# Kernel optimization log

Hardware: AMD Instinct MI355X
Metric: run time of the kernel (lower is better)

Reference implementation:

```python
import jax, jax.numpy as jnp
import numpy as np

B, H, E = 8192, 1024, 8


def setup_inputs() -> dict:
    key = jax.random.key(0)
    ks = jax.random.split(key, 6)
    scale = 0.02  # keep gate/expert logits in a sane range
    return {
        "x": jax.random.normal(ks[0], (B, H), jnp.float32),
        "class_label": jax.random.randint(ks[1], (B,), 0, 2),
        "gate_w": jax.random.normal(ks[2], (E, H), jnp.float32) * scale,
        "w1": jax.random.normal(ks[3], (E, H, H), jnp.float32) * scale,
        "b1": jnp.zeros((E, H), jnp.float32),
        "w2": jax.random.normal(ks[4], (E, H, 2), jnp.float32) * scale,
        "b2": jnp.zeros((E, 2), jnp.float32),
    }


def reference(x, class_label, gate_w, w1, b1, w2, b2):
    num_experts = w1.shape[0]
    # --- router ---
    logits = x @ gate_w.T                              # [B, E]
    routing_prob = jax.nn.softmax(logits, axis=-1)     # [B, E]
    idx = jnp.argmax(routing_prob, axis=-1)            # [B] top-1 expert
    dispatch_onehot = jax.nn.one_hot(idx, num_experts, dtype=jnp.float32)
    balancing_loss = (routing_prob.mean(axis=0) * dispatch_onehot.mean(axis=0)).sum() * num_experts
    router_z_loss = jnp.mean(jax.nn.logsumexp(logits, axis=-1) ** 2)
    # --- experts: compute all experts densely, then select the routed one ---
    h = jax.nn.gelu(jnp.einsum('bh,ehd->bed', x, w1) + b1[None], approximate=False)  # [B, E, H]
    probs = jax.nn.softmax(jnp.einsum('bed,edc->bec', h, w2) + b2[None], axis=-1)    # [B, E, 2]
    expert_out = jnp.take_along_axis(probs, idx[:, None, None], axis=1)[:, 0, :]     # [B, 2]
    # --- straight-through-style weight: value 1, grad flows through p_max ---
    p_max = routing_prob.max(axis=-1)                  # [B]
    weight = p_max + jax.lax.stop_gradient(1.0 - p_max)
    weighted_logits = expert_out * weight[:, None]     # [B, 2]
    # CrossEntropyLoss applied on (already softmaxed) outputs, faithful to source
    logp = jax.nn.log_softmax(weighted_logits, axis=-1)
    ce_loss = -jnp.take_along_axis(logp, class_label[:, None], axis=1).mean()
    loss = ce_loss + 0.01 * balancing_loss + 0.001 * router_z_loss
    return loss
```

## Files before the change

kernel.cpp:

```cpp
#include <hip/hip_runtime.h>
#include <math.h>

#define BQ 8192
#define HD 1024
#define NE 8
#define CAP 1280

#define BM 256
#define BN 128
#define BK 64
#define NRT 5
#define TILES_PER_E 40


#define WS_CURSOR   0
#define WS_TICK     32
#define WS_S        64
#define WS_ZSUM     96
#define WS_CESUM    100
#define WS_ROWLIST  128
#define WS_LOGITS2  41088
#define WS_HEAD     123008
#define WS_XC       123008
#define WS_W1T      10608768

using f32x4  = __attribute__((ext_vector_type(4))) float;

__device__ __forceinline__ float gelu_exact(float v) {
    return 0.5f * v * (1.0f + erff(v * 0.70710678118654752440f));
}

__device__ __forceinline__ unsigned int f4_to_fp8x4(float f0, float f1, float f2, float f3) {
    int lo = __builtin_amdgcn_cvt_pk_fp8_f32(f0, f1, 0, false);
    return (unsigned int)__builtin_amdgcn_cvt_pk_fp8_f32(f2, f3, lo, true);
}

__device__ __forceinline__ void gll16(const void* g, void* l) {
    __builtin_amdgcn_global_load_lds((const __attribute__((address_space(1))) void*)g,
                                     (__attribute__((address_space(3))) void*)l, 16, 0, 0);
}

__global__ __launch_bounds__(256) void prep_kernel(
    const float* __restrict__ x, const float* __restrict__ gate_w,
    const float* __restrict__ w1,
    int* __restrict__ cursor, float* __restrict__ S, float* __restrict__ zsum,
    int* __restrict__ rowlist, unsigned char* __restrict__ xcq,
    unsigned char* __restrict__ w1tq)
{
    __shared__ __align__(16) char smem[33280];
    int tid = threadIdx.x;

    if (blockIdx.x >= 256) {
        char (*lt)[80] = (char (*)[80])smem;
        int tile = blockIdx.x - 256;
        int e = tile >> 8;
        int rem = tile & 255;
        int k0 = (rem >> 4) << 6, n0 = (rem & 15) << 6;
        const float* src = w1 + ((size_t)e << 20) + (size_t)k0 * HD + n0;
        #pragma unroll
        for (int s = 0; s < 4; s++) {
            int q = tid + s * 256;
            int kk = q >> 4, n4 = q & 15;
            float4 v = *(const float4*)(src + (size_t)kk * HD + n4 * 4);
            unsigned int b = f4_to_fp8x4(v.x * 8.f, v.y * 8.f, v.z * 8.f, v.w * 8.f);
            lt[n4 * 4 + 0][kk] = (char)(b);
            lt[n4 * 4 + 1][kk] = (char)(b >> 8);
            lt[n4 * 4 + 2][kk] = (char)(b >> 16);
            lt[n4 * 4 + 3][kk] = (char)(b >> 24);
        }
        __syncthreads();
        int nn = tid >> 2, q = tid & 3;
        int pos0 = ((q & 1) << 5) | ((q >> 1) << 3);
        unsigned char* dst = w1tq + ((size_t)e << 20) + (size_t)(n0 + nn) * HD + k0;
        const unsigned long long* sp = (const unsigned long long*)&lt[nn][q * 16];
        *(unsigned long long*)(dst + pos0)      = sp[0];
        *(unsigned long long*)(dst + pos0 + 16) = sp[1];
        return;
    }

    float* gw    = (float*)smem;
    float* sS    = (float*)(smem + 32768);
    float* sZ    = (float*)(smem + 32800);
    int*   sBI   = (int*)(smem + 32832);
    int*   sSlot = (int*)(smem + 32960);
    int*   sBase = (int*)(smem + 33088);

    for (int i = tid * 4; i < NE * HD; i += 256 * 4) {
        *(float4*)(gw + i) = *(const float4*)(gate_w + i);
    }
    if (tid < NE) sS[tid] = 0.f;
    if (tid == 0) sZ[0] = 0.f;
    __syncthreads();

    int wave = tid >> 6, lane = tid & 63;
    int r0 = blockIdx.x * 32;
    float accS[NE];
    #pragma unroll
    for (int e = 0; e < NE; e++) accS[e] = 0.f;
    float accZ = 0.f;

    #pragma unroll 1
    for (int i = 0; i < 8; i++) {
        int li = wave * 8 + i;
        int r = r0 + li;
        const float* xr = x + (size_t)r * HD;
        float acc[NE];
        #pragma unroll
        for (int e = 0; e < NE; e++) acc[e] = 0.f;
        #pragma unroll
        for (int it = 0; it < 4; it++) {
            int k = lane * 4 + it * 256;
            float4 xv = *(const float4*)(xr + k);
            #pragma unroll
            for (int e = 0; e < NE; e++) {
                const float* g = gw + e * HD + k;
                acc[e] += xv.x * g[0] + xv.y * g[1] + xv.z * g[2] + xv.w * g[3];
            }
        }
        #pragma unroll
        for (int e = 0; e < NE; e++) {
            #pragma unroll
            for (int off = 32; off > 0; off >>= 1)
                acc[e] += __shfl_xor(acc[e], off);
        }
        if (lane == 0) {
            float m = acc[0]; int bi = 0;
            #pragma unroll
            for (int e = 1; e < NE; e++) if (acc[e] > m) { m = acc[e]; bi = e; }
            float se = 0.f, ex[NE];
            #pragma unroll
            for (int e = 0; e < NE; e++) { ex[e] = expf(acc[e] - m); se += ex[e]; }
            float inv = 1.f / se;
            #pragma unroll
            for (int e = 0; e < NE; e++) accS[e] += ex[e] * inv;
            float lse = m + logf(se);
            accZ += lse * lse;
            sBI[li] = bi;
        }
    }
    if (lane == 0) {
        #pragma unroll
        for (int e = 0; e < NE; e++) atomicAdd(&sS[e], accS[e]);
        atomicAdd(sZ, accZ);
    }
    __syncthreads();

    if (tid < NE) {
        int cnt = 0;
        #pragma unroll
        for (int j = 0; j < 32; j++) cnt += (sBI[j] == tid);
        sBase[tid] = atomicAdd(&cursor[tid], cnt);
        atomicAdd(&S[tid], sS[tid]);
    }
    if (tid == 0) atomicAdd(zsum, sZ[0]);
    __syncthreads();

    if (tid < 32) {
        int bi = sBI[tid];
        int rank = 0;
        for (int j = 0; j < tid; j++) rank += (sBI[j] == bi);
        int slot = sBase[bi] + rank;
        sSlot[tid] = slot;
        if (slot < CAP) rowlist[bi * CAP + slot] = r0 + tid;
    }
    __syncthreads();

    #pragma unroll 1
    for (int i = 0; i < 8; i++) {
        int li = wave * 8 + i;
        int bi = sBI[li];
        int pos = sSlot[li];
        if (pos >= CAP) continue;
        const float* src = x + (size_t)(r0 + li) * HD + lane * 16;
        float4 v0 = *(const float4*)(src + 0);
        float4 v1 = *(const float4*)(src + 4);
        float4 v2 = *(const float4*)(src + 8);
        float4 v3 = *(const float4*)(src + 12);
        unsigned int g0a = f4_to_fp8x4(v0.x, v0.y, v0.z, v0.w);
        unsigned int g0b = f4_to_fp8x4(v1.x, v1.y, v1.z, v1.w);
        unsigned int g1a = f4_to_fp8x4(v2.x, v2.y, v2.z, v2.w);
        unsigned int g1b = f4_to_fp8x4(v3.x, v3.y, v3.z, v3.w);
        int s = lane >> 2, q = lane & 3;
        int pos0 = (s << 6) | ((q & 1) << 5) | ((q >> 1) << 3);
        unsigned char* dst = xcq + ((size_t)(bi * CAP + pos)) * HD;
        *(unsigned long long*)(dst + pos0)      = (unsigned long long)g0a | ((unsigned long long)g0b << 32);
        *(unsigned long long*)(dst + pos0 + 16) = (unsigned long long)g1a | ((unsigned long long)g1b << 32);
    }
}

__global__ __launch_bounds__(512, 4) void expert_gemm_kernel(
    const unsigned char* __restrict__ xcq, const unsigned char* __restrict__ w1tq,
    const float* __restrict__ b1, const float* __restrict__ w2,
    const int* __restrict__ cursor, int* __restrict__ tick,
    float* __restrict__ logits2c)
{
    int e = blockIdx.x & 7;
    int cnt = cursor[e]; if (cnt > CAP) cnt = CAP;

    __shared__ __align__(16) char lds[3][24576];
    __shared__ int sTix;

    int t = threadIdx.x;
    int l = t & 63;
    int scolb = ((t & 3) ^ ((t >> 3) & 3)) << 4;
    int m = t >> 2;

    int wid = t >> 6;
    int wr = wid >> 1, wc = wid & 1;
    int r = l & 15, h = l >> 4;
    int off = (h << 4) ^ (((r >> 1) & 3) << 4);

    const unsigned char* xcp  = xcq + ((size_t)e * CAP) * HD;
    const unsigned char* w1tp = w1tq + ((size_t)e << 20);

    for (;;) {
        if (t == 0) sTix = atomicAdd(&tick[e], 1);
        __syncthreads();
        int tix = sTix;
        if (tix >= TILES_PER_E) break;
        int col = tix / NRT;
        int rt = tix - col * NRT;
        if (rt * BM >= cnt) continue;
        int n0 = col * BN;

        const unsigned char* srcA  = xcp + (size_t)(rt * BM + m) * HD + scolb;
        const unsigned char* srcA1 = srcA + (size_t)128 * HD;
        const unsigned char* srcB  = w1tp + (size_t)(n0 + m) * HD + scolb;

        f32x4 acc[4][4];
        #pragma unroll
        for (int i = 0; i < 4; i++)
            #pragma unroll
            for (int j = 0; j < 4; j++) acc[i][j] = (f32x4)(0.f);

        auto stage = [&](int bi) {
            gll16(srcA,  lds[bi] + t * 16);         srcA  += BK;
            gll16(srcA1, lds[bi] + 8192 + t * 16);  srcA1 += BK;
            gll16(srcB,  lds[bi] + 16384 + t * 16); srcB  += BK;
        };
        auto compute = [&](int bi) {
            const char* Ar = lds[bi] + (wr * 64 + r) * 64 + off;
            const char* Br = lds[bi] + 16384 + (wc * 64 + r) * 64 + off;
            longlong2 av[4], bv[4];
            #pragma unroll
            for (int i = 0; i < 4; i++) {
                av[i] = *(const longlong2*)(Ar + i * 1024);
                bv[i] = *(const longlong2*)(Br + i * 1024);
            }
            #pragma unroll
            for (int i = 0; i < 4; i++)
                #pragma unroll
                for (int j = 0; j < 4; j++)
                    acc[i][j] = __builtin_amdgcn_mfma_f32_16x16x32_fp8_fp8(av[i].x, bv[j].x, acc[i][j], 0, 0, 0);
            #pragma unroll
            for (int i = 0; i < 4; i++)
                #pragma unroll
                for (int j = 0; j < 4; j++)
                    acc[i][j] = __builtin_amdgcn_mfma_f32_16x16x32_fp8_fp8(av[i].y, bv[j].y, acc[i][j], 0, 0, 0);
        };

        stage(0); stage(1);
        int cs = 2, cc = 0;
        #pragma unroll 1
        for (int it = 0; it < HD / BK - 2; ++it) {
            asm volatile("s_waitcnt vmcnt(3)" ::: "memory");
            __builtin_amdgcn_s_barrier();
            stage(cs); cs = (cs == 2) ? 0 : cs + 1;
            compute(cc); cc = (cc == 2) ? 0 : cc + 1;
        }
        asm volatile("s_waitcnt vmcnt(3)" ::: "memory");
        __builtin_amdgcn_s_barrier();
        compute(cc); cc = (cc == 2) ? 0 : cc + 1;
        asm volatile("s_waitcnt vmcnt(0)" ::: "memory");
        __builtin_amdgcn_s_barrier();
        compute(cc);

        float b1v[4], w20v[4], w21v[4];
        #pragma unroll
        for (int j = 0; j < 4; j++) {
            int cj = n0 + wc * 64 + j * 16 + r;
            b1v[j]  = b1[e * HD + cj];
            w20v[j] = w2[((size_t)e * HD + cj) * 2 + 0];
            w21v[j] = w2[((size_t)e * HD + cj) * 2 + 1];
        }
        #pragma unroll
        for (int i = 0; i < 4; i++) {
            #pragma unroll
            for (int reg = 0; reg < 4; reg++) {
                float s0 = 0.f, s1 = 0.f;
                #pragma unroll
                for (int j = 0; j < 4; j++) {
                    float hv = gelu_exact(acc[i][j][reg] * 0.125f + b1v[j]);
                    s0 += hv * w20v[j];
                    s1 += hv * w21v[j];
                }
                #pragma unroll
                for (int offx = 1; offx < 16; offx <<= 1) {
                    s0 += __shfl_xor(s0, offx);
                    s1 += __shfl_xor(s1, offx);
                }
                if (r == 0) {
                    int lm = wr * 64 + i * 16 + 4 * h + reg;
                    int p = rt * BM + lm;
                    if (p < cnt) {
                        atomicAdd(&logits2c[(e * CAP + p) * 2 + 0], s0);
                        atomicAdd(&logits2c[(e * CAP + p) * 2 + 1], s1);
                    }
                }
            }
        }
    }
}

__global__ __launch_bounds__(256) void ce_kernel(
    const float* __restrict__ logits2c, const float* __restrict__ b2,
    const int* __restrict__ cursor, const int* __restrict__ rowlist,
    const int* __restrict__ label, float* __restrict__ cesum)
{
    __shared__ float red[4];
    int tid = threadIdx.x;
    int s = blockIdx.x * 256 + tid;
    int e = s / CAP;
    int local = s - e * CAP;
    int cnt = cursor[e]; if (cnt > CAP) cnt = CAP;
    float ce = 0.f;
    if (local < cnt) {
        int rr = rowlist[s];
        float l0 = logits2c[s * 2 + 0] + b2[e * 2 + 0];
        float l1 = logits2c[s * 2 + 1] + b2[e * 2 + 1];
        float mx = fmaxf(l0, l1);
        float e0 = expf(l0 - mx), e1 = expf(l1 - mx);
        float inv = 1.f / (e0 + e1);
        float p0 = e0 * inv, p1 = e1 * inv;
        float m2 = fmaxf(p0, p1);
        float z = m2 + logf(expf(p0 - m2) + expf(p1 - m2));
        float lp = ((label[rr] == 0) ? p0 : p1) - z;
        ce = -lp;
    }
    int lane = tid & 63, wave = tid >> 6;
    #pragma unroll
    for (int off = 32; off > 0; off >>= 1) ce += __shfl_xor(ce, off);
    if (lane == 0) red[wave] = ce;
    __syncthreads();
    if (tid == 0) atomicAdd(cesum, red[0] + red[1] + red[2] + red[3]);
}

__global__ void finalize_kernel(const float* __restrict__ S, const int* __restrict__ cursor,
                                const float* __restrict__ zsum, const float* __restrict__ cesum,
                                float* __restrict__ out)
{
    if (threadIdx.x == 0 && blockIdx.x == 0) {
        float bal = 0.f;
        for (int e = 0; e < NE; e++) bal += S[e] * (float)cursor[e];
        bal *= (float)NE / ((float)BQ * (float)BQ);
        out[0] = cesum[0] / (float)BQ + 0.01f * bal + 0.001f * (zsum[0] / (float)BQ);
    }
}

extern "C" void kernel_launch(void* const* d_in, const int* in_sizes, int n_in,
                              void* d_out, int out_size, void* d_ws, size_t ws_size,
                              hipStream_t stream) {
    const float* x      = (const float*)d_in[0];
    const int*   label  = (const int*)d_in[1];
    const float* gate_w = (const float*)d_in[2];
    const float* w1     = (const float*)d_in[3];
    const float* b1     = (const float*)d_in[4];
    const float* w2     = (const float*)d_in[5];
    const float* b2     = (const float*)d_in[6];
    float* out = (float*)d_out;

    char* ws = (char*)d_ws;
    int*   cursor   = (int*)(ws + WS_CURSOR);
    int*   tick     = (int*)(ws + WS_TICK);
    float* S        = (float*)(ws + WS_S);
    float* zsum     = (float*)(ws + WS_ZSUM);
    float* cesum    = (float*)(ws + WS_CESUM);
    int*   rowlist  = (int*)(ws + WS_ROWLIST);
    float* logits2c = (float*)(ws + WS_LOGITS2);
    unsigned char* xcq  = (unsigned char*)(ws + WS_XC);
    unsigned char* w1tq = (unsigned char*)(ws + WS_W1T);

    hipMemsetAsync(d_ws, 0, WS_HEAD, stream);

    prep_kernel<<<2304, 256, 0, stream>>>(x, gate_w, w1, cursor, S, zsum,
                                          rowlist, xcq, w1tq);
    expert_gemm_kernel<<<512, 512, 0, stream>>>(xcq, w1tq, b1, w2, cursor, tick,
                                                logits2c);
    ce_kernel<<<NE * CAP / 256, 256, 0, stream>>>(logits2c, b2, cursor, rowlist,
                                                  label, cesum);
    finalize_kernel<<<1, 64, 0, stream>>>(S, cursor, zsum, cesum, out);
}
```

Measured before the change: 85.71 us.

## Replace persistent atomic tile scheduler with static 128x128 tiles per block

The expert GEMM's row tile shrinks from 256 to 128 and each block drops from 512 to 256 threads. The persistent loop that claimed tiles through an atomic ticket counter is replaced by a static grid of one block per (expert, tile), with blocks that fall past the expert's row count exiting early. This removes the per-tile atomic and barrier and gives finer-grained load balance when experts have uneven row counts. In exchange, each tile reuses less of the loaded data and more blocks must be launched.

```diff
diff --git a/kernel.cpp b/kernel.cpp
--- a/kernel.cpp
+++ b/kernel.cpp
@@ -6,15 +6,15 @@
 #define NE 8
 #define CAP 1280
 
-#define BM 256
+#define BM 128
 #define BN 128
 #define BK 64
-#define NRT 5
-#define TILES_PER_E 40
+#define NRT 10
+#define NCT 8
+#define TILES_PER_E 80
 
 
 #define WS_CURSOR   0
-#define WS_TICK     32
 #define WS_S        64
 #define WS_ZSUM     96
 #define WS_CESUM    100
@@ -188,17 +188,21 @@
     }
 }
 
-__global__ __launch_bounds__(512, 4) void expert_gemm_kernel(
+__global__ __launch_bounds__(256, 3) void expert_gemm_kernel(
     const unsigned char* __restrict__ xcq, const unsigned char* __restrict__ w1tq,
     const float* __restrict__ b1, const float* __restrict__ w2,
-    const int* __restrict__ cursor, int* __restrict__ tick,
-    float* __restrict__ logits2c)
+    const int* __restrict__ cursor, float* __restrict__ logits2c)
 {
-    int e = blockIdx.x & 7;
+    int bid = blockIdx.x;
+    int e = bid & 7;
+    int tix = bid >> 3;
+    int col = tix / NRT;
+    int rt = tix - col * NRT;
     int cnt = cursor[e]; if (cnt > CAP) cnt = CAP;
-
-    __shared__ __align__(16) char lds[3][24576];
-    __shared__ int sTix;
+    if (rt * BM >= cnt) return;
+    int n0 = col * BN;
+
+    __shared__ __align__(16) char lds[3][16384];
 
     int t = threadIdx.x;
     int l = t & 63;
@@ -213,99 +217,89 @@
     const unsigned char* xcp  = xcq + ((size_t)e * CAP) * HD;
     const unsigned char* w1tp = w1tq + ((size_t)e << 20);
 
-    for (;;) {
-        if (t == 0) sTix = atomicAdd(&tick[e], 1);
-        __syncthreads();
-        int tix = sTix;
-        if (tix >= TILES_PER_E) break;
-        int col = tix / NRT;
-        int rt = tix - col * NRT;
-        if (rt * BM >= cnt) continue;
-        int n0 = col * BN;
-
-        const unsigned char* srcA  = xcp + (size_t)(rt * BM + m) * HD + scolb;
-        const unsigned char* srcA1 = srcA + (size_t)128 * HD;
-        const unsigned char* srcB  = w1tp + (size_t)(n0 + m) * HD + scolb;
-
-        f32x4 acc[4][4];
+    const unsigned char* srcA0 = xcp + (size_t)(rt * BM + m) * HD + scolb;
+    const unsigned char* srcA1 = srcA0 + (size_t)64 * HD;
+    const unsigned char* srcB0 = w1tp + (size_t)(n0 + m) * HD + scolb;
+    const unsigned char* srcB1 = srcB0 + (size_t)64 * HD;
+
+    f32x4 acc[4][4];
+    #pragma unroll
+    for (int i = 0; i < 4; i++)
+        #pragma unroll
+        for (int j = 0; j < 4; j++) acc[i][j] = (f32x4)(0.f);
+
+    auto stage = [&](int bi) {
+        gll16(srcA0, lds[bi] + t * 16);         srcA0 += BK;
+        gll16(srcA1, lds[bi] + 4096 + t * 16);  srcA1 += BK;
+        gll16(srcB0, lds[bi] + 8192 + t * 16);  srcB0 += BK;
+        gll16(srcB1, lds[bi] + 12288 + t * 16); srcB1 += BK;
+    };
+    auto compute = [&](int bi) {
+        const char* Ar = lds[bi] + (wr * 64 + r) * 64 + off;
+        const char* Br = lds[bi] + 8192 + (wc * 64 + r) * 64 + off;
+        longlong2 av[4], bv[4];
+        #pragma unroll
+        for (int i = 0; i < 4; i++) {
+            av[i] = *(const longlong2*)(Ar + i * 1024);
+            bv[i] = *(const longlong2*)(Br + i * 1024);
+        }
         #pragma unroll
         for (int i = 0; i < 4; i++)
             #pragma unroll
-            for (int j = 0; j < 4; j++) acc[i][j] = (f32x4)(0.f);
-
-        auto stage = [&](int bi) {
-            gll16(srcA,  lds[bi] + t * 16);         srcA  += BK;
-            gll16(srcA1, lds[bi] + 8192 + t * 16);  srcA1 += BK;
-            gll16(srcB,  lds[bi] + 16384 + t * 16); srcB  += BK;
-        };
-        auto compute = [&](int bi) {
-            const char* Ar = lds[bi] + (wr * 64 + r) * 64 + off;
-            const char* Br = lds[bi] + 16384 + (wc * 64 + r) * 64 + off;
-            longlong2 av[4], bv[4];
-            #pragma unroll
-            for (int i = 0; i < 4; i++) {
-                av[i] = *(const longlong2*)(Ar + i * 1024);
-                bv[i] = *(const longlong2*)(Br + i * 1024);
+            for (int j = 0; j < 4; j++)
+                acc[i][j] = __builtin_amdgcn_mfma_f32_16x16x32_fp8_fp8(av[i].x, bv[j].x, acc[i][j], 0, 0, 0);
+        #pragma unroll
+        for (int i = 0; i < 4; i++)
+            #pragma unroll
+            for (int j = 0; j < 4; j++)
+                acc[i][j] = __builtin_amdgcn_mfma_f32_16x16x32_fp8_fp8(av[i].y, bv[j].y, acc[i][j], 0, 0, 0);
+    };
+
+    stage(0); stage(1);
+    int cs = 2, cc = 0;
+    #pragma unroll 1
+    for (int it = 0; it < HD / BK - 2; ++it) {
+        asm volatile("s_waitcnt vmcnt(4)" ::: "memory");
+        __builtin_amdgcn_s_barrier();
+        stage(cs); cs = (cs == 2) ? 0 : cs + 1;
+        compute(cc); cc = (cc == 2) ? 0 : cc + 1;
+    }
+    asm volatile("s_waitcnt vmcnt(4)" ::: "memory");
+    __builtin_amdgcn_s_barrier();
+    compute(cc); cc = (cc == 2) ? 0 : cc + 1;
+    asm volatile("s_waitcnt vmcnt(0)" ::: "memory");
+    __builtin_amdgcn_s_barrier();
+    compute(cc);
+
+    float b1v[4], w20v[4], w21v[4];
+    #pragma unroll
+    for (int j = 0; j < 4; j++) {
+        int cj = n0 + wc * 64 + j * 16 + r;
+        b1v[j]  = b1[e * HD + cj];
+        w20v[j] = w2[((size_t)e * HD + cj) * 2 + 0];
+        w21v[j] = w2[((size_t)e * HD + cj) * 2 + 1];
+    }
+    #pragma unroll
+    for (int i = 0; i < 4; i++) {
+        #pragma unroll
+        for (int reg = 0; reg < 4; reg++) {
+            float s0 = 0.f, s1 = 0.f;
+            #pragma unroll
+            for (int j = 0; j < 4; j++) {
+                float hv = gelu_exact(acc[i][j][reg] * 0.125f + b1v[j]);
+                s0 += hv * w20v[j];
+                s1 += hv * w21v[j];
             }
             #pragma unroll
-            for (int i = 0; i < 4; i++)
-                #pragma unroll
-                for (int j = 0; j < 4; j++)
-                    acc[i][j] = __builtin_amdgcn_mfma_f32_16x16x32_fp8_fp8(av[i].x, bv[j].x, acc[i][j], 0, 0, 0);
-            #pragma unroll
-            for (int i = 0; i < 4; i++)
-                #pragma unroll
-                for (int j = 0; j < 4; j++)
-                    acc[i][j] = __builtin_amdgcn_mfma_f32_16x16x32_fp8_fp8(av[i].y, bv[j].y, acc[i][j], 0, 0, 0);
-        };
-
-        stage(0); stage(1);
-        int cs = 2, cc = 0;
-        #pragma unroll 1
-        for (int it = 0; it < HD / BK - 2; ++it) {
-            asm volatile("s_waitcnt vmcnt(3)" ::: "memory");
-            __builtin_amdgcn_s_barrier();
-            stage(cs); cs = (cs == 2) ? 0 : cs + 1;
-            compute(cc); cc = (cc == 2) ? 0 : cc + 1;
-        }
-        asm volatile("s_waitcnt vmcnt(3)" ::: "memory");
-        __builtin_amdgcn_s_barrier();
-        compute(cc); cc = (cc == 2) ? 0 : cc + 1;
-        asm volatile("s_waitcnt vmcnt(0)" ::: "memory");
-        __builtin_amdgcn_s_barrier();
-        compute(cc);
-
-        float b1v[4], w20v[4], w21v[4];
-        #pragma unroll
-        for (int j = 0; j < 4; j++) {
-            int cj = n0 + wc * 64 + j * 16 + r;
-            b1v[j]  = b1[e * HD + cj];
-            w20v[j] = w2[((size_t)e * HD + cj) * 2 + 0];
-            w21v[j] = w2[((size_t)e * HD + cj) * 2 + 1];
-        }
-        #pragma unroll
-        for (int i = 0; i < 4; i++) {
-            #pragma unroll
-            for (int reg = 0; reg < 4; reg++) {
-                float s0 = 0.f, s1 = 0.f;
-                #pragma unroll
-                for (int j = 0; j < 4; j++) {
-                    float hv = gelu_exact(acc[i][j][reg] * 0.125f + b1v[j]);
-                    s0 += hv * w20v[j];
-                    s1 += hv * w21v[j];
-                }
-                #pragma unroll
-                for (int offx = 1; offx < 16; offx <<= 1) {
-                    s0 += __shfl_xor(s0, offx);
-                    s1 += __shfl_xor(s1, offx);
-                }
-                if (r == 0) {
-                    int lm = wr * 64 + i * 16 + 4 * h + reg;
-                    int p = rt * BM + lm;
-                    if (p < cnt) {
-                        atomicAdd(&logits2c[(e * CAP + p) * 2 + 0], s0);
-                        atomicAdd(&logits2c[(e * CAP + p) * 2 + 1], s1);
-                    }
+            for (int offx = 1; offx < 16; offx <<= 1) {
+                s0 += __shfl_xor(s0, offx);
+                s1 += __shfl_xor(s1, offx);
+            }
+            if (r == 0) {
+                int p = rt * BM + wr * 64 + i * 16 + 4 * h + reg;
+                if (p < cnt) {
+                    atomicAdd(&logits2c[(e * CAP + p) * 2 + 0], s0);
+                    atomicAdd(&logits2c[(e * CAP + p) * 2 + 1], s1);
                 }
             }
         }
@@ -371,7 +365,6 @@
 
     char* ws = (char*)d_ws;
     int*   cursor   = (int*)(ws + WS_CURSOR);
-    int*   tick     = (int*)(ws + WS_TICK);
     float* S        = (float*)(ws + WS_S);
     float* zsum     = (float*)(ws + WS_ZSUM);
     float* cesum    = (float*)(ws + WS_CESUM);
@@ -384,8 +377,8 @@
 
     prep_kernel<<<2304, 256, 0, stream>>>(x, gate_w, w1, cursor, S, zsum,
                                           rowlist, xcq, w1tq);
-    expert_gemm_kernel<<<512, 512, 0, stream>>>(xcq, w1tq, b1, w2, cursor, tick,
-                                                logits2c);
+    expert_gemm_kernel<<<NE * TILES_PER_E, 256, 0, stream>>>(xcq, w1tq, b1, w2,
+                                                             cursor, logits2c);
     ce_kernel<<<NE * CAP / 256, 256, 0, stream>>>(logits2c, b2, cursor, rowlist,
                                                   label, cesum);
     finalize_kernel<<<1, 64, 0, stream>>>(S, cursor, zsum, cesum, out);
```

Result: faster. 73.29 us (-14.5%).
